# Performance work log

Measured on AMD Instinct MI355X. Metric: run time of the kernel, lower is better.

Reference implementation:

```python
import jax, jax.numpy as jnp
import numpy as np

B, S_ENC, T_DEC, I, H = 1024, 49, 25, 76, 2048  # S_ENC = source_seq_len - 1


def setup_inputs() -> dict:
    key = jax.random.key(0)
    ks = jax.random.split(key, 6)
    sc = 0.02
    return {
        "encoder_inputs": jax.random.normal(ks[0], (B, S_ENC, I), jnp.float32),
        "decoder_inputs": jax.random.normal(ks[1], (B, T_DEC, I), jnp.float32),
        "W_ih": jax.random.normal(ks[2], (3 * H, I), jnp.float32) * sc,
        "W_hh": jax.random.normal(ks[3], (3 * H, H), jnp.float32) * sc,
        "b_ih": jnp.zeros((3 * H,), jnp.float32),
        "b_hh": jnp.zeros((3 * H,), jnp.float32),
        "fc_w": jax.random.normal(ks[4], (I, H), jnp.float32) * sc,
        "fc_b": jnp.zeros((I,), jnp.float32),
    }


def gru_cell(x, h, W_ih, W_hh, b_ih, b_hh):
    # PyTorch GRUCell: gates stacked [r; z; n] along first axis of weights.
    gi = x @ W_ih.T + b_ih  # [B, 3H]
    gh = h @ W_hh.T + b_hh  # [B, 3H]
    i_r, i_z, i_n = jnp.split(gi, 3, axis=-1)
    h_r, h_z, h_n = jnp.split(gh, 3, axis=-1)
    r = jax.nn.sigmoid(i_r + h_r)
    z = jax.nn.sigmoid(i_z + h_z)
    n = jnp.tanh(i_n + r * h_n)
    return (1.0 - z) * n + z * h


def reference(encoder_inputs, decoder_inputs, W_ih, W_hh, b_ih, b_hh, fc_w, fc_b):
    # Dropout p=0.0 (and eval mode) -> identity; omitted.
    h0 = jnp.zeros((encoder_inputs.shape[0], H), encoder_inputs.dtype)
    enc = jnp.swapaxes(encoder_inputs, 0, 1)  # [S_ENC, B, I]

    def enc_step(h, x):
        return gru_cell(x, h, W_ih, W_hh, b_ih, b_hh), None

    h, _ = jax.lax.scan(enc_step, h0, enc)

    # Sampling-based decoding: only decoder_inputs[:, 0] is consumed; every
    # later step feeds back the previous output. Each step's input is detached.
    prev0 = decoder_inputs[:, 0, :]

    def dec_step(carry, _):
        h, prev = carry
        inp = jax.lax.stop_gradient(prev)  # inp.detach() in the torch code
        h_new = gru_cell(inp, h, W_ih, W_hh, b_ih, b_hh)
        out = inp + h_new @ fc_w.T + fc_b  # residual over fc1 projection
        return (h_new, out), out

    _, outs = jax.lax.scan(dec_step, (h, prev0), None, length=T_DEC)
    return jnp.swapaxes(outs, 0, 1)  # [B, T_DEC, I]
```

## Files before the change

### kernel.cpp

```cpp
#include <hip/hip_runtime.h>
#include <cstdint>
#include <cstddef>

#define DI __device__ __forceinline__

typedef __bf16 bf16x8 __attribute__((ext_vector_type(8)));
typedef float  f32x4  __attribute__((ext_vector_type(4)));
typedef unsigned short ushort_t;

constexpr int BATCH = 1024;
constexpr int HID   = 2048;
constexpr int IN    = 76;
constexpr int SENC  = 49;
constexpr int TDEC  = 25;
constexpr int KX    = 128;
constexpr int KP    = KX + HID;
constexpr int BK    = 64;
constexpr int KTT   = KP / BK;
constexpr int OSTR  = TDEC * IN;

DI unsigned short f2bf(float f) {
  union { float f; unsigned u; } v; v.f = f;
  unsigned u = v.u;
  return (unsigned short)((u + 0x7fffu + ((u >> 16) & 1u)) >> 16);
}

DI f32x4 mfma16(bf16x8 a, bf16x8 b, f32x4 c) {
  return __builtin_amdgcn_mfma_f32_16x16x32_bf16(a, b, c, 0, 0, 0);
}

DI void gload_lds16(const void* g, void* l) {
  __builtin_amdgcn_global_load_lds((const __attribute__((address_space(1))) void*)g,
                                   (__attribute__((address_space(3))) void*)l,
                                   16, 0, 0);
}

DI float sigmoidf_(float x) { return 1.0f / (1.0f + __expf(-x)); }
DI float tanhf_(float x)    { return 1.0f - 2.0f / (1.0f + __expf(2.0f * x)); }


__global__ void pack_W(const float* __restrict__ Wih, const float* __restrict__ Whh,
                       ushort_t* __restrict__ Wp) {
  int idx = blockIdx.x * 256 + threadIdx.x;
  if (idx >= 6144 * KP) return;
  int n = idx / KP;
  int k = idx - n * KP;
  float v = 0.f;
  if (k < IN)        v = Wih[(size_t)n * IN + k];
  else if (k >= KX)  v = Whh[(size_t)n * HID + (k - KX)];
  Wp[idx] = f2bf(v);
}

__global__ void pack_xe(const float* __restrict__ enc, ushort_t* __restrict__ xe) {
  int idx = blockIdx.x * 256 + threadIdx.x;
  if (idx >= SENC * BATCH * KX) return;
  int t = idx >> 17;
  int rem = idx & 131071;
  int b = rem >> 7, k = rem & 127;
  float v = (k < IN) ? enc[(size_t)b * (SENC * IN) + t * IN + k] : 0.f;
  xe[idx] = f2bf(v);
}

__global__ void pack_xd0(const float* __restrict__ dec, ushort_t* __restrict__ xd) {
  int idx = blockIdx.x * 256 + threadIdx.x;
  if (idx >= BATCH * KX) return;
  int b = idx >> 7, k = idx & 127;
  float v = (k < IN) ? dec[(size_t)b * OSTR + k] : 0.f;
  xd[idx] = f2bf(v);
}

__global__ void pack_fc(const float* __restrict__ fcw, ushort_t* __restrict__ Wfc) {
  int idx = blockIdx.x * 256 + threadIdx.x;
  if (idx >= 80 * HID) return;
  int n = idx >> 11, k = idx & 2047;
  float v = (n < IN) ? fcw[(size_t)n * HID + k] : 0.f;
  Wfc[idx] = f2bf(v);
}

__global__ __launch_bounds__(512, 2) void gru_step_kernel(
    const ushort_t* __restrict__ x,
    const ushort_t* __restrict__ hbp,
    const float*    __restrict__ hfp,
    const ushort_t* __restrict__ Wp,
    const float*    __restrict__ b_ih,
    const float*    __restrict__ b_hh,
    float*          __restrict__ hfn,
    ushort_t*       __restrict__ hbn)
{
  __shared__ ushort_t lds[3][(128 + 192) * BK];

  const int tid  = threadIdx.x;
  const int lane = tid & 63;
  const int wid  = tid >> 6;
  const int bid  = blockIdx.x;
  const int n_grp = (bid & 7) + 8 * (bid >> 6);
  const int m_grp = (bid >> 3) & 7;
  const int row0  = m_grp * 128;
  const int col0  = n_grp * 64;
  const int wm = wid >> 1, wn = wid & 1;

  const int srow  = lane >> 3;
  const int swcol = (((lane & 7) ^ (srow & 7)) << 3);

  const f32x4 Z4 = {0.f, 0.f, 0.f, 0.f};
  f32x4 accr[2][2], accz[2][2], accin[2][2], accN[2][2];
  #pragma unroll
  for (int a = 0; a < 2; ++a)
    #pragma unroll
    for (int b = 0; b < 2; ++b) { accr[a][b] = Z4; accz[a][b] = Z4; accin[a][b] = Z4; accN[a][b] = Z4; }

  const int lr  = lane & 15;
  const int bc  = (lane >> 4) * 16;
  const int ksw0 = ((bc)      ^ ((lane & 7) << 4)) >> 1;
  const int ksw1 = ((64 + bc) ^ ((lane & 7) << 4)) >> 1;

  auto stage = [&](int buf, int kt) {
    const ushort_t* asrc; int astr, ak0;
    if (kt < 2) { asrc = x;   astr = KX;  ak0 = kt * BK; }
    else        { asrc = hbp; astr = HID; ak0 = (kt - 2) * BK; }
    ushort_t* Lb = &lds[buf][0];
    #pragma unroll
    for (int c = 0; c < 2; ++c) {
      const int chunk = wid * 2 + c;
      const ushort_t* g = asrc + (size_t)(row0 + chunk * 8 + srow) * astr + ak0 + swcol;
      gload_lds16(g, Lb + chunk * 512);
    }
    const int wk0 = kt * BK;
    #pragma unroll
    for (int c = 0; c < 3; ++c) {
      const int chunk = wid * 3 + c;
      const int brow = chunk * 8 + srow;
      const int gg = brow >> 6, wi = brow & 63;
      const ushort_t* g = Wp + (size_t)(gg * HID + col0 + wi) * KP + wk0 + swcol;
      gload_lds16(g, Lb + 128 * BK + chunk * 512);
    }
  };

  auto readFrags = [&](const ushort_t* base, int ko, bf16x8 af[2], bf16x8 bg[3][2]) {
    const ushort_t* Ab = base;
    const ushort_t* Bb = base + 128 * BK;
    #pragma unroll
    for (int fm = 0; fm < 2; ++fm)
      af[fm] = *reinterpret_cast<const bf16x8*>(&Ab[(wm * 32 + fm * 16 + lr) * BK + ko]);
    #pragma unroll
    for (int g = 0; g < 3; ++g)
      #pragma unroll
      for (int fn = 0; fn < 2; ++fn)
        bg[g][fn] = *reinterpret_cast<const bf16x8*>(&Bb[(g * 64 + wn * 32 + fn * 16 + lr) * BK + ko]);
  };

  auto burst = [&](bf16x8 af[2], bf16x8 bg[3][2]) {
    __builtin_amdgcn_s_setprio(1);
    #pragma unroll
    for (int fm = 0; fm < 2; ++fm)
      #pragma unroll
      for (int fn = 0; fn < 2; ++fn) {
        accr[fm][fn] = mfma16(af[fm], bg[0][fn], accr[fm][fn]);
        accz[fm][fn] = mfma16(af[fm], bg[1][fn], accz[fm][fn]);
        accN[fm][fn] = mfma16(af[fm], bg[2][fn], accN[fm][fn]);
      }
    __builtin_amdgcn_s_setprio(0);
  };

  stage(0, 0);
  stage(1, 1);
  asm volatile("s_waitcnt vmcnt(5)" ::: "memory");
  __builtin_amdgcn_s_barrier();

  bf16x8 afA[2], bgA[3][2];
  bf16x8 afB[2], bgB[3][2];
  readFrags(&lds[0][0], ksw0, afA, bgA);

  for (int kt = 0; kt < KTT - 1; ++kt) {
    const ushort_t* cur = &lds[kt % 3][0];
    readFrags(cur, ksw1, afB, bgB);
    burst(afA, bgA);

    asm volatile("s_waitcnt vmcnt(0)" ::: "memory");
    __builtin_amdgcn_s_barrier();
    if (kt + 2 < KTT) stage((kt + 2) % 3, kt + 2);

    readFrags(&lds[(kt + 1) % 3][0], ksw0, afA, bgA);
    burst(afB, bgB);

    if (kt == 1) {
      #pragma unroll
      for (int a = 0; a < 2; ++a)
        #pragma unroll
        for (int b = 0; b < 2; ++b) { accin[a][b] = accN[a][b]; accN[a][b] = Z4; }
    }
  }
  {
    const ushort_t* cur = &lds[(KTT - 1) % 3][0];
    readFrags(cur, ksw1, afB, bgB);
    burst(afA, bgA);
    burst(afB, bgB);
  }

  const int lqb = (lane >> 4) * 4;
  #pragma unroll
  for (int fn = 0; fn < 2; ++fn) {
    const int j = col0 + wn * 32 + fn * 16 + lr;
    const float br  = b_ih[j] + b_hh[j];
    const float bz  = b_ih[HID + j] + b_hh[HID + j];
    const float bin = b_ih[2 * HID + j];
    const float bhn = b_hh[2 * HID + j];
    #pragma unroll
    for (int fm = 0; fm < 2; ++fm) {
      #pragma unroll
      for (int q = 0; q < 4; ++q) {
        const int row = row0 + wm * 32 + fm * 16 + lqb + q;
        const size_t off = (size_t)row * HID + j;
        const float hp = hfp[off];
        const float rr = sigmoidf_(accr[fm][fn][q] + br);
        const float zz = sigmoidf_(accz[fm][fn][q] + bz);
        const float nn = tanhf_(accin[fm][fn][q] + bin + rr * (accN[fm][fn][q] + bhn));
        const float hv = (1.0f - zz) * nn + zz * hp;
        hfn[off] = hv;
        hbn[off] = f2bf(hv);
      }
    }
  }
}

__global__ __launch_bounds__(256) void fc_kernel(
    const ushort_t* __restrict__ hb,
    const ushort_t* __restrict__ Wfc,
    const float*    __restrict__ fc_b,
    const float*    __restrict__ prev,
    float*          __restrict__ outp,
    ushort_t*       __restrict__ xd)
{
  __shared__ float red[4][16][80];
  const int tid = threadIdx.x, lane = tid & 63, wid = tid >> 6;
  const int r0 = blockIdx.x * 16;
  const int lr = lane & 15, lk = (lane >> 4) * 8;
  const f32x4 Z4 = {0.f, 0.f, 0.f, 0.f};
  f32x4 acc[5];
  #pragma unroll
  for (int f = 0; f < 5; ++f) acc[f] = Z4;
  const int kbase = wid * 512;
  #pragma unroll
  for (int ks = 0; ks < 16; ++ks) {
    const int k = kbase + ks * 32 + lk;
    bf16x8 a = *reinterpret_cast<const bf16x8*>(&hb[(size_t)(r0 + lr) * HID + k]);
    #pragma unroll
    for (int f = 0; f < 5; ++f) {
      bf16x8 b = *reinterpret_cast<const bf16x8*>(&Wfc[(size_t)(f * 16 + lr) * HID + k]);
      acc[f] = mfma16(a, b, acc[f]);
    }
  }
  #pragma unroll
  for (int f = 0; f < 5; ++f)
    #pragma unroll
    for (int q = 0; q < 4; ++q)
      red[wid][(lane >> 4) * 4 + q][f * 16 + lr] = acc[f][q];
  __syncthreads();

  const int rowi = tid >> 4;
  const int j0   = (tid & 15) * 8;
  const int b_   = r0 + rowi;
  #pragma unroll
  for (int jj = 0; jj < 8; ++jj) {
    const int j = j0 + jj;
    float ov = 0.f;
    if (j < IN) {
      float s = red[0][rowi][j] + red[1][rowi][j] + red[2][rowi][j] + red[3][rowi][j];
      ov = prev[(size_t)b_ * OSTR + j] + fc_b[j] + s;
      outp[(size_t)b_ * OSTR + j] = ov;
    }
    xd[b_ * KX + j] = f2bf(j < IN ? ov : 0.f);
  }
}

extern "C" void kernel_launch(void* const* d_in, const int* in_sizes, int n_in,
                              void* d_out, int out_size, void* d_ws, size_t ws_size,
                              hipStream_t stream) {
  const float* enc = (const float*)d_in[0];
  const float* dec = (const float*)d_in[1];
  const float* Wih = (const float*)d_in[2];
  const float* Whh = (const float*)d_in[3];
  const float* bih = (const float*)d_in[4];
  const float* bhh = (const float*)d_in[5];
  const float* fcw = (const float*)d_in[6];
  const float* fcb = (const float*)d_in[7];
  float* out = (float*)d_out;

  char* ws = (char*)d_ws;
  ushort_t* Wp  = (ushort_t*)ws;  ws += (size_t)6144 * KP * 2;
  ushort_t* xe  = (ushort_t*)ws;  ws += (size_t)SENC * BATCH * KX * 2;
  ushort_t* xd  = (ushort_t*)ws;  ws += (size_t)BATCH * KX * 2;
  ushort_t* Wfc = (ushort_t*)ws;  ws += (size_t)80 * HID * 2;
  float* hf0 = (float*)ws;        ws += (size_t)BATCH * HID * 4;
  float* hf1 = (float*)ws;        ws += (size_t)BATCH * HID * 4;
  ushort_t* hb0 = (ushort_t*)ws;  ws += (size_t)BATCH * HID * 2;
  ushort_t* hb1 = (ushort_t*)ws;  ws += (size_t)BATCH * HID * 2;
  float* hf[2] = {hf0, hf1};
  ushort_t* hbp[2] = {hb0, hb1};

  pack_W  <<<(6144 * KP + 255) / 256, 256, 0, stream>>>(Wih, Whh, Wp);
  pack_xe <<<(SENC * BATCH * KX + 255) / 256, 256, 0, stream>>>(enc, xe);
  pack_xd0<<<(BATCH * KX + 255) / 256, 256, 0, stream>>>(dec, xd);
  pack_fc <<<(80 * HID + 255) / 256, 256, 0, stream>>>(fcw, Wfc);
  hipMemsetAsync(hf0, 0, (size_t)BATCH * HID * 4, stream);
  hipMemsetAsync(hb0, 0, (size_t)BATCH * HID * 2, stream);

  for (int s = 0; s < SENC + TDEC; ++s) {
    const ushort_t* xsrc = (s < SENC) ? (xe + (size_t)s * BATCH * KX) : xd;
    gru_step_kernel<<<256, 512, 0, stream>>>(xsrc, hbp[s & 1], hf[s & 1], Wp, bih, bhh,
                                             hf[(s + 1) & 1], hbp[(s + 1) & 1]);
    if (s >= SENC) {
      const int t = s - SENC;
      const float* prev = (t == 0) ? dec : (out + (size_t)(t - 1) * IN);
      fc_kernel<<<64, 256, 0, stream>>>(hbp[(s + 1) & 1], Wfc, fcb, prev,
                                        out + (size_t)t * IN, xd);
    }
  }
}
```

Before: 2.733 ms.

## Drop fp32 hidden state, re-tile warps 2x4, restructure LDS pipeline

```diff
diff --git a/kernel.cpp b/kernel.cpp
--- a/kernel.cpp
+++ b/kernel.cpp
@@ -25,6 +25,11 @@
   return (unsigned short)((u + 0x7fffu + ((u >> 16) & 1u)) >> 16);
 }
 
+DI float bf2f(unsigned short h) {
+  union { unsigned u; float f; } v; v.u = ((unsigned)h) << 16;
+  return v.f;
+}
+
 DI f32x4 mfma16(bf16x8 a, bf16x8 b, f32x4 c) {
   return __builtin_amdgcn_mfma_f32_16x16x32_bf16(a, b, c, 0, 0, 0);
 }
@@ -80,11 +85,9 @@
 __global__ __launch_bounds__(512, 2) void gru_step_kernel(
     const ushort_t* __restrict__ x,
     const ushort_t* __restrict__ hbp,
-    const float*    __restrict__ hfp,
     const ushort_t* __restrict__ Wp,
     const float*    __restrict__ b_ih,
     const float*    __restrict__ b_hh,
-    float*          __restrict__ hfn,
     ushort_t*       __restrict__ hbn)
 {
   __shared__ ushort_t lds[3][(128 + 192) * BK];
@@ -97,17 +100,16 @@
   const int m_grp = (bid >> 3) & 7;
   const int row0  = m_grp * 128;
   const int col0  = n_grp * 64;
-  const int wm = wid >> 1, wn = wid & 1;
+  const int wm = wid >> 2;
+  const int wn = wid & 3;
+
+  const f32x4 Z4 = {0.f, 0.f, 0.f, 0.f};
+  f32x4 accr[4], accz[4], accN[4], accin[4];
+  #pragma unroll
+  for (int a = 0; a < 4; ++a) { accr[a] = Z4; accz[a] = Z4; accN[a] = Z4; accin[a] = Z4; }
 
   const int srow  = lane >> 3;
   const int swcol = (((lane & 7) ^ (srow & 7)) << 3);
-
-  const f32x4 Z4 = {0.f, 0.f, 0.f, 0.f};
-  f32x4 accr[2][2], accz[2][2], accin[2][2], accN[2][2];
-  #pragma unroll
-  for (int a = 0; a < 2; ++a)
-    #pragma unroll
-    for (int b = 0; b < 2; ++b) { accr[a][b] = Z4; accz[a][b] = Z4; accin[a][b] = Z4; accN[a][b] = Z4; }
 
   const int lr  = lane & 15;
   const int bc  = (lane >> 4) * 16;
@@ -136,89 +138,73 @@
     }
   };
 
-  auto readFrags = [&](const ushort_t* base, int ko, bf16x8 af[2], bf16x8 bg[3][2]) {
-    const ushort_t* Ab = base;
-    const ushort_t* Bb = base + 128 * BK;
-    #pragma unroll
-    for (int fm = 0; fm < 2; ++fm)
-      af[fm] = *reinterpret_cast<const bf16x8*>(&Ab[(wm * 32 + fm * 16 + lr) * BK + ko]);
+  auto readFrags = [&](const ushort_t* base, int ko, bf16x8 af[4], bf16x8 bg[3]) {
+    #pragma unroll
+    for (int fm = 0; fm < 4; ++fm)
+      af[fm] = *reinterpret_cast<const bf16x8*>(&base[(wm * 64 + fm * 16 + lr) * BK + ko]);
     #pragma unroll
     for (int g = 0; g < 3; ++g)
-      #pragma unroll
-      for (int fn = 0; fn < 2; ++fn)
-        bg[g][fn] = *reinterpret_cast<const bf16x8*>(&Bb[(g * 64 + wn * 32 + fn * 16 + lr) * BK + ko]);
+      bg[g] = *reinterpret_cast<const bf16x8*>(
+          &base[128 * BK + (g * 64 + wn * 16 + lr) * BK + ko]);
   };
 
-  auto burst = [&](bf16x8 af[2], bf16x8 bg[3][2]) {
+  auto burst = [&](bf16x8 af[4], bf16x8 bg[3]) {
     __builtin_amdgcn_s_setprio(1);
     #pragma unroll
-    for (int fm = 0; fm < 2; ++fm)
-      #pragma unroll
-      for (int fn = 0; fn < 2; ++fn) {
-        accr[fm][fn] = mfma16(af[fm], bg[0][fn], accr[fm][fn]);
-        accz[fm][fn] = mfma16(af[fm], bg[1][fn], accz[fm][fn]);
-        accN[fm][fn] = mfma16(af[fm], bg[2][fn], accN[fm][fn]);
-      }
+    for (int fm = 0; fm < 4; ++fm) {
+      accr[fm] = mfma16(af[fm], bg[0], accr[fm]);
+      accz[fm] = mfma16(af[fm], bg[1], accz[fm]);
+      accN[fm] = mfma16(af[fm], bg[2], accN[fm]);
+    }
     __builtin_amdgcn_s_setprio(0);
   };
+
+  bf16x8 afA[4], bgA[3];
+  bf16x8 afB[4], bgB[3];
 
   stage(0, 0);
   stage(1, 1);
   asm volatile("s_waitcnt vmcnt(5)" ::: "memory");
   __builtin_amdgcn_s_barrier();
 
-  bf16x8 afA[2], bgA[3][2];
-  bf16x8 afB[2], bgB[3][2];
-  readFrags(&lds[0][0], ksw0, afA, bgA);
-
-  for (int kt = 0; kt < KTT - 1; ++kt) {
-    const ushort_t* cur = &lds[kt % 3][0];
-    readFrags(cur, ksw1, afB, bgB);
+  for (int kt = 0; kt < KTT; ++kt) {
+    const ushort_t* base = &lds[kt % 3][0];
+    readFrags(base, ksw0, afA, bgA);
+    if (kt + 2 < KTT) stage((kt + 2) % 3, kt + 2);
+    readFrags(base, ksw1, afB, bgB);
     burst(afA, bgA);
-
-    asm volatile("s_waitcnt vmcnt(0)" ::: "memory");
-    __builtin_amdgcn_s_barrier();
-    if (kt + 2 < KTT) stage((kt + 2) % 3, kt + 2);
-
-    readFrags(&lds[(kt + 1) % 3][0], ksw0, afA, bgA);
     burst(afB, bgB);
 
     if (kt == 1) {
       #pragma unroll
-      for (int a = 0; a < 2; ++a)
-        #pragma unroll
-        for (int b = 0; b < 2; ++b) { accin[a][b] = accN[a][b]; accN[a][b] = Z4; }
-    }
-  }
-  {
-    const ushort_t* cur = &lds[(KTT - 1) % 3][0];
-    readFrags(cur, ksw1, afB, bgB);
-    burst(afA, bgA);
-    burst(afB, bgB);
+      for (int a = 0; a < 4; ++a) { accin[a] = accN[a]; accN[a] = Z4; }
+    }
+
+    if (kt + 1 < KTT) {
+      if (kt + 2 < KTT) { asm volatile("s_waitcnt vmcnt(5)" ::: "memory"); }
+      else              { asm volatile("s_waitcnt vmcnt(0)" ::: "memory"); }
+      __builtin_amdgcn_s_barrier();
+    }
   }
 
   const int lqb = (lane >> 4) * 4;
-  #pragma unroll
-  for (int fn = 0; fn < 2; ++fn) {
-    const int j = col0 + wn * 32 + fn * 16 + lr;
-    const float br  = b_ih[j] + b_hh[j];
-    const float bz  = b_ih[HID + j] + b_hh[HID + j];
-    const float bin = b_ih[2 * HID + j];
-    const float bhn = b_hh[2 * HID + j];
-    #pragma unroll
-    for (int fm = 0; fm < 2; ++fm) {
-      #pragma unroll
-      for (int q = 0; q < 4; ++q) {
-        const int row = row0 + wm * 32 + fm * 16 + lqb + q;
-        const size_t off = (size_t)row * HID + j;
-        const float hp = hfp[off];
-        const float rr = sigmoidf_(accr[fm][fn][q] + br);
-        const float zz = sigmoidf_(accz[fm][fn][q] + bz);
-        const float nn = tanhf_(accin[fm][fn][q] + bin + rr * (accN[fm][fn][q] + bhn));
-        const float hv = (1.0f - zz) * nn + zz * hp;
-        hfn[off] = hv;
-        hbn[off] = f2bf(hv);
-      }
+  const int j = col0 + wn * 16 + lr;
+  const float br  = b_ih[j] + b_hh[j];
+  const float bz  = b_ih[HID + j] + b_hh[HID + j];
+  const float bin = b_ih[2 * HID + j];
+  const float bhn = b_hh[2 * HID + j];
+  #pragma unroll
+  for (int fm = 0; fm < 4; ++fm) {
+    #pragma unroll
+    for (int q = 0; q < 4; ++q) {
+      const int row = row0 + wm * 64 + fm * 16 + lqb + q;
+      const size_t off = (size_t)row * HID + j;
+      const float hp = bf2f(hbp[off]);
+      const float rr = sigmoidf_(accr[fm][q] + br);
+      const float zz = sigmoidf_(accz[fm][q] + bz);
+      const float nn = tanhf_(accin[fm][q] + bin + rr * (accN[fm][q] + bhn));
+      const float hv = (1.0f - zz) * nn + zz * hp;
+      hbn[off] = f2bf(hv);
     }
   }
 }
@@ -291,24 +277,20 @@
   ushort_t* xe  = (ushort_t*)ws;  ws += (size_t)SENC * BATCH * KX * 2;
   ushort_t* xd  = (ushort_t*)ws;  ws += (size_t)BATCH * KX * 2;
   ushort_t* Wfc = (ushort_t*)ws;  ws += (size_t)80 * HID * 2;
-  float* hf0 = (float*)ws;        ws += (size_t)BATCH * HID * 4;
-  float* hf1 = (float*)ws;        ws += (size_t)BATCH * HID * 4;
   ushort_t* hb0 = (ushort_t*)ws;  ws += (size_t)BATCH * HID * 2;
   ushort_t* hb1 = (ushort_t*)ws;  ws += (size_t)BATCH * HID * 2;
-  float* hf[2] = {hf0, hf1};
   ushort_t* hbp[2] = {hb0, hb1};
 
   pack_W  <<<(6144 * KP + 255) / 256, 256, 0, stream>>>(Wih, Whh, Wp);
   pack_xe <<<(SENC * BATCH * KX + 255) / 256, 256, 0, stream>>>(enc, xe);
   pack_xd0<<<(BATCH * KX + 255) / 256, 256, 0, stream>>>(dec, xd);
   pack_fc <<<(80 * HID + 255) / 256, 256, 0, stream>>>(fcw, Wfc);
-  hipMemsetAsync(hf0, 0, (size_t)BATCH * HID * 4, stream);
   hipMemsetAsync(hb0, 0, (size_t)BATCH * HID * 2, stream);
 
   for (int s = 0; s < SENC + TDEC; ++s) {
     const ushort_t* xsrc = (s < SENC) ? (xe + (size_t)s * BATCH * KX) : xd;
-    gru_step_kernel<<<256, 512, 0, stream>>>(xsrc, hbp[s & 1], hf[s & 1], Wp, bih, bhh,
-                                             hf[(s + 1) & 1], hbp[(s + 1) & 1]);
+    gru_step_kernel<<<256, 512, 0, stream>>>(xsrc, hbp[s & 1], Wp, bih, bhh,
+                                             hbp[(s + 1) & 1]);
     if (s >= SENC) {
       const int t = s - SENC;
       const float* prev = (t == 0) ? dec : (out + (size_t)(t - 1) * IN);
```

New measurement: 2.691 ms. About the same (-1.5%).
